# Kernel tuning notes

Hardware: AMD Instinct MI355X
Metric: run time of the kernel (lower is better)

Reference implementation:

```python
import jax, jax.numpy as jnp
import numpy as np

D_MODEL = 1024
HIDDEN = 512
NUM_EXPERTS = 16
TOP_K = 2
CAP_FACTOR = 1.25
ALPHA = 0.01


def setup_inputs() -> dict:
    key = jax.random.key(0)
    ks = jax.random.split(key, 10)
    s_in = 1.0 / np.sqrt(D_MODEL)
    s_h = 1.0 / np.sqrt(HIDDEN)
    return {
        "x": jax.random.normal(ks[0], (4, 4096, D_MODEL), dtype=jnp.float32),
        "gate_w": jax.random.normal(ks[1], (D_MODEL, NUM_EXPERTS), dtype=jnp.float32) * s_in,
        "gate_b": jnp.zeros((NUM_EXPERTS,), dtype=jnp.float32),
        "gp_w": jax.random.normal(ks[2], (NUM_EXPERTS, D_MODEL, HIDDEN), dtype=jnp.float32) * s_in,
        "gp_b": jnp.zeros((NUM_EXPERTS, HIDDEN), dtype=jnp.float32),
        "up_w": jax.random.normal(ks[3], (NUM_EXPERTS, D_MODEL, HIDDEN), dtype=jnp.float32) * s_in,
        "up_b": jnp.zeros((NUM_EXPERTS, HIDDEN), dtype=jnp.float32),
        "dp_w": jax.random.normal(ks[4], (NUM_EXPERTS, HIDDEN, D_MODEL), dtype=jnp.float32) * s_h,
        "dp_b": jnp.zeros((NUM_EXPERTS, D_MODEL), dtype=jnp.float32),
    }


def reference(x, gate_w, gate_b, gp_w, gp_b, up_w, up_b, dp_w, dp_b):
    B, S, D = x.shape
    T = B * S
    xf = x.reshape(T, D)

    # --- MoEGate ---
    logits = xf @ gate_w + gate_b                      # [T, E]
    scores = jax.nn.softmax(logits, axis=-1)
    topk_w, topk_i = jax.lax.top_k(scores, TOP_K)      # [T, K]
    # norm_topk_prob=True in DeepSeekMoE
    topk_w = topk_w / (jnp.sum(topk_w, axis=-1, keepdims=True) + 1e-9)

    one_hot = jax.nn.one_hot(topk_i, NUM_EXPERTS, dtype=jnp.float32)  # [T, K, E]
    load = jnp.sum(one_hot, axis=(0, 1))               # [E]
    capacity = CAP_FACTOR * (T * TOP_K) / NUM_EXPERTS
    capacity_penalty = jnp.sum(jax.nn.relu(load - capacity)) / NUM_EXPERTS / T
    aux_loss = ALPHA * capacity_penalty

    # combine weight of expert e for each token: [T, E]
    comb = jnp.einsum("tke,tk->te", one_hot, topk_w)

    # --- dispatch/combine (dense per-expert, weighted by comb) ---
    out = jnp.zeros_like(xf)
    for e in range(NUM_EXPERTS):
        # Expert: down_proj(gate_proj(x) * silu(up_proj(x)))
        h = (xf @ gp_w[e] + gp_b[e]) * jax.nn.silu(xf @ up_w[e] + up_b[e])
        y = h @ dp_w[e] + dp_b[e]
        out = out + comb[:, e:e + 1] * y

    return out.reshape(B, S, D), aux_loss
```

## Files before the change

### kernel.cpp

```cpp
#include <hip/hip_runtime.h>
#include <hip/hip_bf16.h>
#include <math.h>

#define T_TOK 16384
#define DMODEL 1024
#define HID 512
#define NEXP 16
#define NASSIGN (T_TOK * 2)
#define HIST_BLK 64
#define TOK_PER_BLK (T_TOK / HIST_BLK)

typedef __bf16 bf16_8 __attribute__((ext_vector_type(8)));
typedef __bf16 bf16_4 __attribute__((ext_vector_type(4)));
typedef float f32_4 __attribute__((ext_vector_type(4)));

__device__ __forceinline__ void gload16(const __bf16* g, __bf16* l) {
  __builtin_amdgcn_global_load_lds(
      (const __attribute__((address_space(1))) void*)g,
      (__attribute__((address_space(3))) void*)l, 16, 0, 0);
}

__global__ __launch_bounds__(256) void gate_compute_kernel(
    const float* __restrict__ x, const float* __restrict__ gw, const float* __restrict__ gb,
    __bf16* __restrict__ xb, int* __restrict__ topk_idx, float2* __restrict__ topk_w)
{
  int wave = threadIdx.x >> 6;
  int lane = threadIdx.x & 63;
  int t = blockIdx.x * 4 + wave;
  const float* xr = x + (size_t)t * DMODEL;
  float acc[NEXP];
#pragma unroll
  for (int e = 0; e < NEXP; ++e) acc[e] = 0.f;
#pragma unroll
  for (int ii = 0; ii < DMODEL / 256; ++ii) {
    int i = ii * 256 + lane * 4;
    f32_4 xv = *(const f32_4*)(xr + i);
    bf16_4 xbv;
#pragma unroll
    for (int j = 0; j < 4; ++j) {
      xbv[j] = (__bf16)xv[j];
      const float* g = gw + (size_t)(i + j) * NEXP;
#pragma unroll
      for (int e = 0; e < NEXP; ++e) acc[e] = fmaf(xv[j], g[e], acc[e]);
    }
    *(bf16_4*)(xb + (size_t)t * DMODEL + i) = xbv;
  }
#pragma unroll
  for (int e = 0; e < NEXP; ++e) {
    float v = acc[e];
#pragma unroll
    for (int s = 32; s > 0; s >>= 1) v += __shfl_xor(v, s, 64);
    acc[e] = v;
  }
  if (lane == 0) {
    float mx = -1e30f;
#pragma unroll
    for (int e = 0; e < NEXP; ++e) { acc[e] += gb[e]; mx = fmaxf(mx, acc[e]); }
    float Z = 0.f;
#pragma unroll
    for (int e = 0; e < NEXP; ++e) { acc[e] = expf(acc[e] - mx); Z += acc[e]; }
    int i0 = 0; float s0 = acc[0];
#pragma unroll
    for (int e = 1; e < NEXP; ++e) if (acc[e] > s0) { s0 = acc[e]; i0 = e; }
    int i1 = -1; float s1 = -1e30f;
#pragma unroll
    for (int e = 0; e < NEXP; ++e) if (e != i0 && acc[e] > s1) { s1 = acc[e]; i1 = e; }
    s0 /= Z; s1 /= Z;
    float dn = s0 + s1 + 1e-9f;
    topk_idx[t] = i0 | (i1 << 8);
    topk_w[t] = make_float2(s0 / dn, s1 / dn);
  }
}

__global__ __launch_bounds__(256) void hist_kernel(
    const int* __restrict__ topk_idx, int* __restrict__ block_hist)
{
  __shared__ int cnt[NEXP];
  int tid = threadIdx.x;
  if (tid < NEXP) cnt[tid] = 0;
  __syncthreads();
  int t = blockIdx.x * TOK_PER_BLK + tid;
  int p = topk_idx[t];
  atomicAdd(&cnt[p & 0xff], 1);
  atomicAdd(&cnt[p >> 8], 1);
  __syncthreads();
  if (tid < NEXP) block_hist[blockIdx.x * NEXP + tid] = cnt[tid];
}

__global__ void scan2_kernel(const int* __restrict__ block_hist,
                             int* __restrict__ counts, int* __restrict__ offsets,
                             int* __restrict__ block_base, float* __restrict__ aux_out)
{
  __shared__ int cl[NEXP];
  int lane = threadIdx.x;
  if (lane < NEXP) {
    int s = 0;
    for (int b = 0; b < HIST_BLK; ++b) s += block_hist[b * NEXP + lane];
    cl[lane] = s;
    counts[lane] = s;
  }
  __syncthreads();
  if (lane < NEXP) {
    int off = 0;
    for (int e = 0; e < lane; ++e) off += cl[e];
    offsets[lane] = off;
    int base = off;
    for (int b = 0; b < HIST_BLK; ++b) {
      block_base[b * NEXP + lane] = base;
      base += block_hist[b * NEXP + lane];
    }
  }
  if (lane == 0) {
    int tot = 0; float pen = 0.f;
    const float cap = 1.25f * (float)(T_TOK * 2) / (float)NEXP;
    for (int e = 0; e < NEXP; ++e) {
      tot += cl[e];
      float ld = (float)cl[e] - cap;
      pen += ld > 0.f ? ld : 0.f;
    }
    offsets[NEXP] = tot;
    aux_out[0] = 0.01f * pen / (float)NEXP / (float)T_TOK;
  }
}

__global__ __launch_bounds__(256) void scatter_kernel(
    const int* __restrict__ topk_idx, const int* __restrict__ block_base,
    int* __restrict__ tok_list, int2* __restrict__ tok_slots)
{
  __shared__ int base[NEXP];
  int tid = threadIdx.x;
  if (tid < NEXP) base[tid] = block_base[blockIdx.x * NEXP + tid];
  __syncthreads();
  int t = blockIdx.x * TOK_PER_BLK + tid;
  int p = topk_idx[t];
  int i0 = p & 0xff, i1 = p >> 8;
  int p0 = atomicAdd(&base[i0], 1);
  tok_list[p0] = t;
  int p1 = atomicAdd(&base[i1], 1);
  tok_list[p1] = t;
  tok_slots[t] = make_int2(p0, p1);
}

__global__ __launch_bounds__(256) void transpose_w1_kernel(const float* __restrict__ gp,
                                                           const float* __restrict__ up,
                                                           __bf16* __restrict__ wb1)
{
  __shared__ float tile[32][33];
  int ez = blockIdx.z;
  int e = ez >> 1, isup = ez & 1;
  const float* in = isup ? up : gp;
  int c0 = blockIdx.x * 32, r0 = blockIdx.y * 32;
  const float* src = in + ((size_t)e * 1024 + r0) * 512 + c0;
#pragma unroll
  for (int i = 0; i < 4; ++i) {
    int r = threadIdx.y + i * 8;
    tile[r][threadIdx.x] = src[(size_t)r * 512 + threadIdx.x];
  }
  __syncthreads();
#pragma unroll
  for (int i = 0; i < 4; ++i) {
    int cc = threadIdx.y + i * 8;
    int np = 2 * c0 + 2 * (cc & ~15) + (cc & 15) + 16 * isup;
    wb1[((size_t)e * 1024 + np) * 1024 + r0 + threadIdx.x] = (__bf16)tile[threadIdx.x][cc];
  }
}

__global__ __launch_bounds__(256) void transpose_dp_kernel(const float* __restrict__ in,
                                                           __bf16* __restrict__ out)
{
  __shared__ float tile[32][33];
  int e = blockIdx.z;
  int c0 = blockIdx.x * 32, r0 = blockIdx.y * 32;
  const float* src = in + ((size_t)e * 512 + r0) * 1024 + c0;
#pragma unroll
  for (int i = 0; i < 4; ++i) {
    int r = threadIdx.y + i * 8;
    tile[r][threadIdx.x] = src[(size_t)r * 1024 + threadIdx.x];
  }
  __syncthreads();
  __bf16* dst = out + ((size_t)e * 1024 + c0) * 512 + r0;
#pragma unroll
  for (int i = 0; i < 4; ++i) {
    int c = threadIdx.y + i * 8;
    dst[(size_t)c * 512 + threadIdx.x] = (__bf16)tile[threadIdx.x][c];
  }
}


#define PHASE_MID()                                          \
  __builtin_amdgcn_sched_barrier(0);                         \
  __builtin_amdgcn_s_barrier();                              \
  asm volatile("s_waitcnt lgkmcnt(0)" ::: "memory");         \
  __builtin_amdgcn_sched_barrier(0);                         \
  __builtin_amdgcn_s_setprio(1);

#define PHASE_END()                                          \
  __builtin_amdgcn_s_setprio(0);                             \
  __builtin_amdgcn_sched_barrier(0);                         \
  __builtin_amdgcn_s_barrier();

#define KTILE_BODY(STG)                                                           \
  {                                                                               \
    const __bf16* A_ = AsL + cur * 16384;                                         \
    const __bf16* B_ = BsL + cur * 16384;                                         \
    bf16_8 af[8];                                                                 \
    bf16_8 b0, b1;                                                                \
                     \
    _Pragma("unroll")                                                             \
    for (int mi = 0; mi < 8; ++mi)                                                \
      af[mi] = *(const bf16_8*)(A_ + abase + mi * 1024 + c0);                     \
    b0 = *(const bf16_8*)(B_ + bbase + c0);                                       \
    b1 = *(const bf16_8*)(B_ + bbase + 1024 + c0);                                \
    if (STG) {                                                                    \
      gload16(ga0 + koff, AsL + nxt * 16384 + tid * 8);                           \
      gload16(ga1 + koff, AsL + nxt * 16384 + 4096 + tid * 8);                    \
      gload16(ga2 + koff, AsL + nxt * 16384 + 8192 + tid * 8);                    \
      gload16(ga3 + koff, AsL + nxt * 16384 + 12288 + tid * 8);                   \
    }                                                                             \
    PHASE_MID();                                                                  \
    _Pragma("unroll")                                                             \
    for (int mi = 0; mi < 8; ++mi) {                                              \
      acc[mi][0] = __builtin_amdgcn_mfma_f32_16x16x32_bf16(af[mi], b0, acc[mi][0], 0, 0, 0); \
      acc[mi][1] = __builtin_amdgcn_mfma_f32_16x16x32_bf16(af[mi], b1, acc[mi][1], 0, 0, 0); \
    }                                                                             \
    PHASE_END();                                                                  \
                                       \
    b0 = *(const bf16_8*)(B_ + bbase + 2048 + c0);                                \
    b1 = *(const bf16_8*)(B_ + bbase + 3072 + c0);                                \
    if (STG) {                                                                    \
      gload16(gb0 + koff, BsL + nxt * 16384 + tid * 8);                           \
      gload16(gb1 + koff, BsL + nxt * 16384 + 4096 + tid * 8);                    \
      gload16(gb2 + koff, BsL + nxt * 16384 + 8192 + tid * 8);                    \
      gload16(gb3 + koff, BsL + nxt * 16384 + 12288 + tid * 8);                   \
    }                                                                             \
    PHASE_MID();                                                                  \
    _Pragma("unroll")                                                             \
    for (int mi = 0; mi < 8; ++mi) {                                              \
      acc[mi][2] = __builtin_amdgcn_mfma_f32_16x16x32_bf16(af[mi], b0, acc[mi][2], 0, 0, 0); \
      acc[mi][3] = __builtin_amdgcn_mfma_f32_16x16x32_bf16(af[mi], b1, acc[mi][3], 0, 0, 0); \
    }                                                                             \
    PHASE_END();                                                                  \
                                     \
    _Pragma("unroll")                                                             \
    for (int mi = 0; mi < 8; ++mi)                                                \
      af[mi] = *(const bf16_8*)(A_ + abase + mi * 1024 + (c0 ^ 32));              \
    b0 = *(const bf16_8*)(B_ + bbase + (c0 ^ 32));                                \
    b1 = *(const bf16_8*)(B_ + bbase + 1024 + (c0 ^ 32));                         \
    PHASE_MID();                                                                  \
    _Pragma("unroll")                                                             \
    for (int mi = 0; mi < 8; ++mi) {                                              \
      acc[mi][0] = __builtin_amdgcn_mfma_f32_16x16x32_bf16(af[mi], b0, acc[mi][0], 0, 0, 0); \
      acc[mi][1] = __builtin_amdgcn_mfma_f32_16x16x32_bf16(af[mi], b1, acc[mi][1], 0, 0, 0); \
    }                                                                             \
    PHASE_END();                                                                  \
          \
    b0 = *(const bf16_8*)(B_ + bbase + 2048 + (c0 ^ 32));                         \
    b1 = *(const bf16_8*)(B_ + bbase + 3072 + (c0 ^ 32));                         \
    if (STG) { asm volatile("s_waitcnt vmcnt(0)" ::: "memory"); }                 \
    PHASE_MID();                                                                  \
    _Pragma("unroll")                                                             \
    for (int mi = 0; mi < 8; ++mi) {                                              \
      acc[mi][2] = __builtin_amdgcn_mfma_f32_16x16x32_bf16(af[mi], b0, acc[mi][2], 0, 0, 0); \
      acc[mi][3] = __builtin_amdgcn_mfma_f32_16x16x32_bf16(af[mi], b1, acc[mi][3], 0, 0, 0); \
    }                                                                             \
    PHASE_END();                                                                  \
  }

template<int KTILES>
__device__ __forceinline__ void gemm8w(
    const __bf16* ga0, const __bf16* ga1, const __bf16* ga2, const __bf16* ga3,
    const __bf16* gb0, const __bf16* gb1, const __bf16* gb2, const __bf16* gb3,
    __bf16* AsL, __bf16* BsL, f32_4 (&acc)[8][4])
{
  int tid = threadIdx.x;
  int wid = tid >> 6, wr = wid >> 2, wc = wid & 3;
  int lane = tid & 63, quad = lane >> 4, l16 = lane & 15;
  int c0 = ((quad ^ (l16 & 7)) * 8);
  int abase = (wr * 128 + l16) * 64;
  int bbase = (wc * 64 + l16) * 64;

  gload16(ga0, AsL + tid * 8);
  gload16(ga1, AsL + 4096 + tid * 8);
  gload16(ga2, AsL + 8192 + tid * 8);
  gload16(ga3, AsL + 12288 + tid * 8);
  gload16(gb0, BsL + tid * 8);
  gload16(gb1, BsL + 4096 + tid * 8);
  gload16(gb2, BsL + 8192 + tid * 8);
  gload16(gb3, BsL + 12288 + tid * 8);
  __syncthreads();

  int cur = 0;
#pragma unroll 1
  for (int kt = 0; kt < KTILES - 1; ++kt) {
    int nxt = cur ^ 1;
    int koff = (kt + 1) * 64;
    KTILE_BODY(1);
    cur = nxt;
  }
  {
    int nxt = 0; int koff = 0;
    KTILE_BODY(0);
  }
}

__global__ __launch_bounds__(512, 2) void ffn1_kernel(
    const __bf16* __restrict__ xb, const __bf16* __restrict__ wb1,
    const float* __restrict__ gp_b, const float* __restrict__ up_b,
    const int* __restrict__ counts, const int* __restrict__ offsets,
    const int* __restrict__ tok_list, __bf16* __restrict__ h)
{
  int e = blockIdx.z;
  int cnt = counts[e];
  int m0 = blockIdx.y * 256;
  if (m0 >= cnt) return;
  int n0 = blockIdx.x * 256;
  int offe = offsets[e];

  __shared__ __align__(16) __bf16 As[2][256 * 64];
  __shared__ __align__(16) __bf16 Bs[2][256 * 64];
  __shared__ int toks[256];

  int tid = threadIdx.x;
  if (tid < 256) {
    int r = m0 + tid;
    toks[tid] = tok_list[offe + (r < cnt ? r : cnt - 1)];
  }
  __syncthreads();

  int rr = tid >> 3;
  int ko = ((tid & 7) ^ (rr & 7)) * 8;

  f32_4 acc[8][4];
  {
    f32_4 z = {0.f, 0.f, 0.f, 0.f};
#pragma unroll
    for (int a = 0; a < 8; ++a)
#pragma unroll
      for (int b = 0; b < 4; ++b) acc[a][b] = z;
  }

  gemm8w<DMODEL / 64>(
      xb + (size_t)toks[rr] * DMODEL + ko,
      xb + (size_t)toks[64 + rr] * DMODEL + ko,
      xb + (size_t)toks[128 + rr] * DMODEL + ko,
      xb + (size_t)toks[192 + rr] * DMODEL + ko,
      wb1 + ((size_t)e * 1024 + n0 + rr) * DMODEL + ko,
      wb1 + ((size_t)e * 1024 + n0 + 64 + rr) * DMODEL + ko,
      wb1 + ((size_t)e * 1024 + n0 + 128 + rr) * DMODEL + ko,
      wb1 + ((size_t)e * 1024 + n0 + 192 + rr) * DMODEL + ko,
      &As[0][0], &Bs[0][0], acc);

  int wid = tid >> 6, wr = wid >> 2, wc = wid & 3;
  int lane = tid & 63, quad = lane >> 4, l16 = lane & 15;

#pragma unroll
  for (int mi = 0; mi < 8; ++mi)
#pragma unroll
    for (int j = 0; j < 2; ++j) {
      int c = (n0 >> 1) + wc * 32 + j * 16 + l16;
      float gbias = gp_b[e * HID + c];
      float ubias = up_b[e * HID + c];
#pragma unroll
      for (int rg = 0; rg < 4; ++rg) {
        int r = m0 + wr * 128 + mi * 16 + quad * 4 + rg;
        if (r < cnt) {
          float g = acc[mi][2 * j][rg] + gbias;
          float u = acc[mi][2 * j + 1][rg] + ubias;
          float sw = u / (1.f + expf(-u));
          h[(size_t)(offe + r) * HID + c] = (__bf16)(g * sw);
        }
      }
    }
}

__global__ __launch_bounds__(512, 2) void ffn2_kernel(
    const __bf16* __restrict__ h, const __bf16* __restrict__ dpb, const float* __restrict__ dp_b,
    const int* __restrict__ counts, const int* __restrict__ offsets,
    __bf16* __restrict__ ybuf)
{
  int e = blockIdx.z;
  int cnt = counts[e];
  int m0 = blockIdx.y * 256;
  if (m0 >= cnt) return;
  int n0 = blockIdx.x * 256;
  int offe = offsets[e];

  __shared__ __align__(16) __bf16 As[2][256 * 64];
  __shared__ __align__(16) __bf16 Bs[2][256 * 64];

  int tid = threadIdx.x;
  int rr = tid >> 3;
  int ko = ((tid & 7) ^ (rr & 7)) * 8;

  int ra0 = m0 + rr;        if (ra0 >= cnt) ra0 = cnt - 1;
  int ra1 = m0 + 64 + rr;   if (ra1 >= cnt) ra1 = cnt - 1;
  int ra2 = m0 + 128 + rr;  if (ra2 >= cnt) ra2 = cnt - 1;
  int ra3 = m0 + 192 + rr;  if (ra3 >= cnt) ra3 = cnt - 1;

  f32_4 acc[8][4];
  {
    f32_4 z = {0.f, 0.f, 0.f, 0.f};
#pragma unroll
    for (int a = 0; a < 8; ++a)
#pragma unroll
      for (int b = 0; b < 4; ++b) acc[a][b] = z;
  }

  gemm8w<HID / 64>(
      h + (size_t)(offe + ra0) * HID + ko,
      h + (size_t)(offe + ra1) * HID + ko,
      h + (size_t)(offe + ra2) * HID + ko,
      h + (size_t)(offe + ra3) * HID + ko,
      dpb + ((size_t)e * DMODEL + n0 + rr) * HID + ko,
      dpb + ((size_t)e * DMODEL + n0 + 64 + rr) * HID + ko,
      dpb + ((size_t)e * DMODEL + n0 + 128 + rr) * HID + ko,
      dpb + ((size_t)e * DMODEL + n0 + 192 + rr) * HID + ko,
      &As[0][0], &Bs[0][0], acc);

  int wid = tid >> 6, wr = wid >> 2, wc = wid & 3;
  int lane = tid & 63, quad = lane >> 4, l16 = lane & 15;

#pragma unroll
  for (int mi = 0; mi < 8; ++mi)
#pragma unroll
    for (int ni = 0; ni < 4; ++ni) {
      int n = n0 + wc * 64 + ni * 16 + l16;
      float bias = dp_b[e * DMODEL + n];
#pragma unroll
      for (int rg = 0; rg < 4; ++rg) {
        int r = m0 + wr * 128 + mi * 16 + quad * 4 + rg;
        if (r < cnt) {
          float v = acc[mi][ni][rg] + bias;
          ybuf[(size_t)(offe + r) * DMODEL + n] = (__bf16)v;
        }
      }
    }
}

__global__ __launch_bounds__(256) void combine_kernel(
    const __bf16* __restrict__ ybuf, const int2* __restrict__ tok_slots,
    const float2* __restrict__ topk_w, float* __restrict__ out)
{
  int tid = threadIdx.x;
  int t = blockIdx.x * 2 + (tid >> 7);
  int d = (tid & 127) * 8;
  int2 sl = tok_slots[t];
  float2 w = topk_w[t];
  bf16_8 y0 = *(const bf16_8*)(ybuf + (size_t)sl.x * DMODEL + d);
  bf16_8 y1 = *(const bf16_8*)(ybuf + (size_t)sl.y * DMODEL + d);
  float* o = out + (size_t)t * DMODEL + d;
  f32_4 r0, r1;
#pragma unroll
  for (int i = 0; i < 4; ++i) r0[i] = w.x * (float)y0[i] + w.y * (float)y1[i];
#pragma unroll
  for (int i = 0; i < 4; ++i) r1[i] = w.x * (float)y0[4 + i] + w.y * (float)y1[4 + i];
  *(f32_4*)o = r0;
  *(f32_4*)(o + 4) = r1;
}

extern "C" void kernel_launch(void* const* d_in, const int* in_sizes, int n_in,
                              void* d_out, int out_size, void* d_ws, size_t ws_size,
                              hipStream_t stream)
{
  const float* x      = (const float*)d_in[0];
  const float* gate_w = (const float*)d_in[1];
  const float* gate_b = (const float*)d_in[2];
  const float* gp_w   = (const float*)d_in[3];
  const float* gp_b   = (const float*)d_in[4];
  const float* up_w   = (const float*)d_in[5];
  const float* up_b   = (const float*)d_in[6];
  const float* dp_w   = (const float*)d_in[7];
  const float* dp_b   = (const float*)d_in[8];

  char* ws = (char*)d_ws;
  size_t o = 0;
  __bf16* xb  = (__bf16*)(ws + o); o += (size_t)T_TOK * DMODEL * 2;
  __bf16* wb1 = (__bf16*)(ws + o); o += (size_t)NEXP * 1024 * DMODEL * 2;
  __bf16* dpb = (__bf16*)(ws + o); o += (size_t)NEXP * DMODEL * HID * 2;
  __bf16* hbuf = (__bf16*)(ws + o); o += (size_t)NASSIGN * HID * 2;
  int*   tok_list = (int*)(ws + o); o += (size_t)NASSIGN * 4;
  int2*  tok_slots = (int2*)(ws + o); o += (size_t)T_TOK * 8;
  int*   topk_idx = (int*)(ws + o); o += (size_t)T_TOK * 4;
  float2* topk_w  = (float2*)(ws + o); o += (size_t)T_TOK * 8;
  int*   block_hist = (int*)(ws + o); o += (size_t)HIST_BLK * NEXP * 4;
  int*   block_base = (int*)(ws + o); o += (size_t)HIST_BLK * NEXP * 4;
  int*   counts   = (int*)(ws + o); o += 64;
  int*   offsets  = (int*)(ws + o); o += 128;
  __bf16* ybuf = (__bf16*)ws;

  float* out = (float*)d_out;
  float* aux = out + (size_t)T_TOK * DMODEL;

  gate_compute_kernel<<<T_TOK / 4, 256, 0, stream>>>(x, gate_w, gate_b, xb, topk_idx, topk_w);
  hist_kernel<<<HIST_BLK, TOK_PER_BLK, 0, stream>>>(topk_idx, block_hist);
  scan2_kernel<<<1, 64, 0, stream>>>(block_hist, counts, offsets, block_base, aux);
  scatter_kernel<<<HIST_BLK, TOK_PER_BLK, 0, stream>>>(topk_idx, block_base, tok_list, tok_slots);
  transpose_w1_kernel<<<dim3(512 / 32, 1024 / 32, 2 * NEXP), dim3(32, 8), 0, stream>>>(gp_w, up_w, wb1);
  transpose_dp_kernel<<<dim3(1024 / 32, 512 / 32, NEXP), dim3(32, 8), 0, stream>>>(dp_w, dpb);
  ffn1_kernel<<<dim3(1024 / 256, NASSIGN / 256, NEXP), 512, 0, stream>>>(xb, wb1, gp_b, up_b,
                                                                         counts, offsets, tok_list, hbuf);
  ffn2_kernel<<<dim3(DMODEL / 256, NASSIGN / 256, NEXP), 512, 0, stream>>>(hbuf, dpb, dp_b,
                                                                           counts, offsets, ybuf);
  combine_kernel<<<T_TOK / 2, 256, 0, stream>>>(ybuf, tok_slots, topk_w, out);
}
```

Measured before the change: 549.5 us.

## Stage gate weights in LDS and compute four tokens per wave in gate kernel

The gate kernel now copies the whole gate weight matrix into shared memory once per block, in an expert-group-major layout. Each wave then processes eight tokens in two passes of four, reusing each LDS weight load across four tokens. Previously every lane read weights from global memory with strided scalar accesses and each wave handled one token. The cost is 64KB of LDS per block, which limits occupancy, plus more registers for the 64 accumulators and extra shuffle reductions.

```diff
diff --git a/kernel.cpp b/kernel.cpp
--- a/kernel.cpp
+++ b/kernel.cpp
@@ -24,51 +24,99 @@
     const float* __restrict__ x, const float* __restrict__ gw, const float* __restrict__ gb,
     __bf16* __restrict__ xb, int* __restrict__ topk_idx, float2* __restrict__ topk_w)
 {
-  int wave = threadIdx.x >> 6;
-  int lane = threadIdx.x & 63;
-  int t = blockIdx.x * 4 + wave;
-  const float* xr = x + (size_t)t * DMODEL;
-  float acc[NEXP];
-#pragma unroll
-  for (int e = 0; e < NEXP; ++e) acc[e] = 0.f;
-#pragma unroll
-  for (int ii = 0; ii < DMODEL / 256; ++ii) {
-    int i = ii * 256 + lane * 4;
-    f32_4 xv = *(const f32_4*)(xr + i);
-    bf16_4 xbv;
-#pragma unroll
-    for (int j = 0; j < 4; ++j) {
-      xbv[j] = (__bf16)xv[j];
-      const float* g = gw + (size_t)(i + j) * NEXP;
-#pragma unroll
-      for (int e = 0; e < NEXP; ++e) acc[e] = fmaf(xv[j], g[e], acc[e]);
-    }
-    *(bf16_4*)(xb + (size_t)t * DMODEL + i) = xbv;
-  }
-#pragma unroll
-  for (int e = 0; e < NEXP; ++e) {
-    float v = acc[e];
-#pragma unroll
-    for (int s = 32; s > 0; s >>= 1) v += __shfl_xor(v, s, 64);
-    acc[e] = v;
-  }
-  if (lane == 0) {
+  __shared__ __align__(16) float gws[4 * 1024 * 4];
+
+  int tid = threadIdx.x;
+#pragma unroll
+  for (int i = 0; i < 16; ++i) {
+    int c = i * 256 + tid;
+    f32_4 v = ((const f32_4*)gw)[c];
+    ((f32_4*)gws)[((c & 3) << 10) | (c >> 2)] = v;
+  }
+  __syncthreads();
+
+  int wave = tid >> 6, lane = tid & 63;
+  int tbase = blockIdx.x * 32 + wave * 8;
+
+#pragma unroll 1
+  for (int pass = 0; pass < 2; ++pass) {
+    int t0 = tbase + pass * 4;
+    const float* xr0 = x + (size_t)t0 * DMODEL;
+    const float* xr1 = xr0 + DMODEL;
+    const float* xr2 = xr1 + DMODEL;
+    const float* xr3 = xr2 + DMODEL;
+    __bf16* xw0 = xb + (size_t)t0 * DMODEL;
+    __bf16* xw1 = xw0 + DMODEL;
+    __bf16* xw2 = xw1 + DMODEL;
+    __bf16* xw3 = xw2 + DMODEL;
+
+    f32_4 acc0[4], acc1[4], acc2[4], acc3[4];
+    {
+      f32_4 z = {0.f, 0.f, 0.f, 0.f};
+#pragma unroll
+      for (int g = 0; g < 4; ++g) { acc0[g] = z; acc1[g] = z; acc2[g] = z; acc3[g] = z; }
+    }
+
+#pragma unroll
+    for (int j = 0; j < 16; ++j) {
+      int k = j * 64 + lane;
+      float xv0 = xr0[k], xv1 = xr1[k], xv2 = xr2[k], xv3 = xr3[k];
+      xw0[k] = (__bf16)xv0;
+      xw1[k] = (__bf16)xv1;
+      xw2[k] = (__bf16)xv2;
+      xw3[k] = (__bf16)xv3;
+      f32_4 w0 = ((const f32_4*)gws)[k];
+      f32_4 w1 = ((const f32_4*)gws)[1024 + k];
+      f32_4 w2 = ((const f32_4*)gws)[2048 + k];
+      f32_4 w3 = ((const f32_4*)gws)[3072 + k];
+      acc0[0] += xv0 * w0; acc0[1] += xv0 * w1; acc0[2] += xv0 * w2; acc0[3] += xv0 * w3;
+      acc1[0] += xv1 * w0; acc1[1] += xv1 * w1; acc1[2] += xv1 * w2; acc1[3] += xv1 * w3;
+      acc2[0] += xv2 * w0; acc2[1] += xv2 * w1; acc2[2] += xv2 * w2; acc2[3] += xv2 * w3;
+      acc3[0] += xv3 * w0; acc3[1] += xv3 * w1; acc3[2] += xv3 * w2; acc3[3] += xv3 * w3;
+    }
+
+#pragma unroll
+    for (int g = 0; g < 4; ++g)
+#pragma unroll
+      for (int w = 0; w < 4; ++w) {
+        float v0 = acc0[g][w], v1 = acc1[g][w], v2 = acc2[g][w], v3 = acc3[g][w];
+#pragma unroll
+        for (int s = 32; s; s >>= 1) {
+          v0 += __shfl_xor(v0, s, 64);
+          v1 += __shfl_xor(v1, s, 64);
+          v2 += __shfl_xor(v2, s, 64);
+          v3 += __shfl_xor(v3, s, 64);
+        }
+        acc0[g][w] = v0; acc1[g][w] = v1; acc2[g][w] = v2; acc3[g][w] = v3;
+      }
+
+    int ti = lane & 3;
+    float sc[16];
+#pragma unroll
+    for (int e = 0; e < 16; ++e) {
+      int g = e >> 2, w = e & 3;
+      float v = ti == 0 ? acc0[g][w] : ti == 1 ? acc1[g][w] : ti == 2 ? acc2[g][w] : acc3[g][w];
+      sc[e] = v + gb[e];
+    }
     float mx = -1e30f;
 #pragma unroll
-    for (int e = 0; e < NEXP; ++e) { acc[e] += gb[e]; mx = fmaxf(mx, acc[e]); }
+    for (int e = 0; e < 16; ++e) mx = fmaxf(mx, sc[e]);
     float Z = 0.f;
 #pragma unroll
-    for (int e = 0; e < NEXP; ++e) { acc[e] = expf(acc[e] - mx); Z += acc[e]; }
-    int i0 = 0; float s0 = acc[0];
-#pragma unroll
-    for (int e = 1; e < NEXP; ++e) if (acc[e] > s0) { s0 = acc[e]; i0 = e; }
+    for (int e = 0; e < 16; ++e) { sc[e] = expf(sc[e] - mx); Z += sc[e]; }
+    int i0 = 0; float s0 = sc[0];
+#pragma unroll
+    for (int e = 1; e < 16; ++e) if (sc[e] > s0) { s0 = sc[e]; i0 = e; }
     int i1 = -1; float s1 = -1e30f;
 #pragma unroll
-    for (int e = 0; e < NEXP; ++e) if (e != i0 && acc[e] > s1) { s1 = acc[e]; i1 = e; }
+    for (int e = 0; e < 16; ++e) if (e != i0 && sc[e] > s1) { s1 = sc[e]; i1 = e; }
     s0 /= Z; s1 /= Z;
     float dn = s0 + s1 + 1e-9f;
-    topk_idx[t] = i0 | (i1 << 8);
-    topk_w[t] = make_float2(s0 / dn, s1 / dn);
+    if (lane < 4) {
+      int t = t0 + ti;
+      topk_idx[t] = i0 | (i1 << 8);
+      topk_w[t] = make_float2(s0 / dn, s1 / dn);
+    }
   }
 }
 
@@ -491,7 +539,7 @@
   float* out = (float*)d_out;
   float* aux = out + (size_t)T_TOK * DMODEL;
 
-  gate_compute_kernel<<<T_TOK / 4, 256, 0, stream>>>(x, gate_w, gate_b, xb, topk_idx, topk_w);
+  gate_compute_kernel<<<T_TOK / 32, 256, 0, stream>>>(x, gate_w, gate_b, xb, topk_idx, topk_w);
   hist_kernel<<<HIST_BLK, TOK_PER_BLK, 0, stream>>>(topk_idx, block_hist);
   scan2_kernel<<<1, 64, 0, stream>>>(block_hist, counts, offsets, block_base, aux);
   scatter_kernel<<<HIST_BLK, TOK_PER_BLK, 0, stream>>>(topk_idx, block_base, tok_list, tok_slots);
```

After: 460.8 us. 16.2% less time.
